# Optimization experiments

Measured on AMD Instinct MI355X. Metric: run time of the kernel, lower is better.

## Reference

```python
import jax, jax.numpy as jnp
import numpy as np

N, E, E_LBL = 50000, 800000, 200000
D_IN, H = 128, 128


def setup_inputs() -> dict:
    key = jax.random.key(0)
    ks = jax.random.split(key, 12)
    s = 0.05
    return {
        "x": jax.random.normal(ks[0], (N, D_IN), jnp.float32),
        "edge_index": jax.random.randint(ks[1], (2, E), 0, N, jnp.int64),
        "edge_label_index": jax.random.randint(ks[2], (2, E_LBL), 0, N, jnp.int64),
        "pre_w": jax.random.normal(ks[3], (D_IN, H), jnp.float32) * s,
        "pre_b": jax.random.normal(ks[4], (H,), jnp.float32) * s,
        "Wx": jax.random.normal(ks[5], (3, 2, H, H), jnp.float32) * s,  # gates z,r,h x cheb orders T0,T1
        "bx": jax.random.normal(ks[6], (3, H), jnp.float32) * s,
        "Wh": jax.random.normal(ks[7], (3, 2, H, H), jnp.float32) * s,
        "bh": jax.random.normal(ks[8], (3, H), jnp.float32) * s,
        "post_w": jax.random.normal(ks[9], (H, 2), jnp.float32) * s,
        "post_b": jax.random.normal(ks[10], (2,), jnp.float32) * s,
    }


def reference(x, edge_index, edge_label_index, pre_w, pre_b, Wx, bx, Wh, bh, post_w, post_b):
    n = x.shape[0]
    src, dst = edge_index[0], edge_index[1]

    # Scaled Chebyshev Laplacian (sym norm, lambda_max=2): L_hat = -D^{-1/2} A D^{-1/2}
    # (diagonal of L_hat is exactly 0, so only off-diagonal edge terms remain).
    deg = jax.ops.segment_sum(jnp.ones_like(src, dtype=x.dtype), src, num_segments=n)
    dinv = jnp.where(deg > 0, jax.lax.rsqrt(jnp.maximum(deg, 1.0)), 0.0)
    w = -(dinv[src] * dinv[dst])  # [E]

    def lap(v):  # L_hat @ v : gather src rows, weight, scatter-add at dst
        return jax.ops.segment_sum(w[:, None] * v[src], dst, num_segments=n)

    def cheb(v, Lv, W2, b):  # ChebConv K=2: T0(v)@W0 + T1(v)@W1 + b
        return v @ W2[0] + Lv @ W2[1] + b

    # pre: Linear(input_dim -> hidden)
    Xh = x @ pre_w + pre_b  # [N, H]
    LX = lap(Xh)

    # GConvGRU single step, H0 = 0
    Hc = jnp.zeros_like(Xh)
    LH = lap(Hc)
    Z = jax.nn.sigmoid(cheb(Xh, LX, Wx[0], bx[0]) + cheb(Hc, LH, Wh[0], bh[0]))
    R = jax.nn.sigmoid(cheb(Xh, LX, Wx[1], bx[1]) + cheb(Hc, LH, Wh[1], bh[1]))
    HR = Hc * R
    LHR = lap(HR)
    Ht = jnp.tanh(cheb(Xh, LX, Wx[2], bx[2]) + cheb(HR, LHR, Wh[2], bh[2]))
    Hc = Z * Hc + (1.0 - Z) * Ht

    h = jax.nn.relu(Hc)
    # link decoder: gather endpoints, hadamard, Linear(H->2), sum over logits
    hprod = h[edge_label_index[0]] * h[edge_label_index[1]]  # [E_lbl, H]
    out = hprod @ post_w + post_b  # [E_lbl, 2]
    return jnp.sum(out, axis=-1)  # [E_lbl]
```

## Files before the change

kernel.cpp:

```cpp
#include <hip/hip_runtime.h>
#include <math.h>


#define RND 2048
#define SORT_CAP 1536
#define CAPB 6144

typedef __attribute__((ext_vector_type(4))) float f32x4;
typedef __attribute__((ext_vector_type(8))) short short8;
typedef __attribute__((ext_vector_type(4))) unsigned u32x4;
typedef __attribute__((ext_vector_type(2))) unsigned u32x2;

static __device__ __forceinline__ unsigned short f2b(float f) {
  union { float f; unsigned u; } v; v.f = f;
  unsigned r = (v.u + 0x7fffu + ((v.u >> 16) & 1u)) >> 16;
  return (unsigned short)r;
}
static __device__ __forceinline__ float b2f(unsigned short s) {
  union { unsigned u; float f; } v; v.u = ((unsigned)s) << 16;
  return v.f;
}
static __device__ __forceinline__ unsigned f2e4m3(float f) {
  unsigned su = (__float_as_uint(f) >> 24) & 0x80u;
  float a = fminf(fabsf(f), 448.0f) * 0x1.0p-120f;
  unsigned u = __float_as_uint(a);
  u += 0x7FFFFu + ((u >> 20) & 1u);
  return su | ((u >> 20) & 0x7Fu);
}
static __device__ __forceinline__ float e4m32f(unsigned b) {
  unsigned u = ((b & 0x80u) << 24) | ((b & 0x7Fu) << 20);
  return __uint_as_float(u) * 0x1.0p120f;
}

__global__ __launch_bounds__(256) void prep_kernel(const float* __restrict__ pre_w, const float* __restrict__ Wx,
                                                   const float* __restrict__ bx, const float* __restrict__ bh,
                                                   const float* __restrict__ post_w, const float* __restrict__ post_b,
                                                   unsigned short* __restrict__ Bt1c, unsigned short* __restrict__ Btc2,
                                                   float* __restrict__ fb2, float* __restrict__ pwsum,
                                                   int* __restrict__ binPos) {
  int e = blockIdx.x * 256 + threadIdx.x;
  if (e < 512) binPos[e * 16] = (e & 255) * CAPB;
  if (e < 16384) {
    int kc = e >> 12, r = e & 4095, col = r >> 5, kk = r & 31;
    Bt1c[e] = f2b(pre_w[(kc * 32 + kk) * 128 + col]);
  }
  int e2 = e - 16384;
  if (e2 >= 0 && e2 < 65536) {
    int kc = e2 >> 13, r = e2 & 8191, cB = r >> 5, kk = r & 31;
    int k = kc * 32 + kk, half = k >> 7, ki = k & 127;
    int cb = cB >> 7, r7 = cB & 127, nw6 = r7 >> 6, u2 = r7 & 63;
    int g = (u2 >= 32) ? 2 : 0, hcol = cb * 64 + nw6 * 32 + (u2 & 31);
    Btc2[e2] = f2b(Wx[((g * 2 + half) * 128 + ki) * 128 + hcol]);
  }
  int e3 = e - (16384 + 65536);
  if (e3 >= 0 && e3 < 256) {
    int cB = e3;
    int cb = cB >> 7, r7 = cB & 127, nw6 = r7 >> 6, u2 = r7 & 63;
    int g = (u2 >= 32) ? 2 : 0, hcol = cb * 64 + nw6 * 32 + (u2 & 31);
    fb2[cB] = bx[g * 128 + hcol] + bh[g * 128 + hcol];
  }
  int e4 = e - (16384 + 65536 + 256);
  if (e4 >= 0 && e4 < 128) pwsum[e4] = post_w[2 * e4] + post_w[2 * e4 + 1];
  if (e4 == 128) pwsum[128] = post_b[0] + post_b[1];
}

union SMemU {
  struct { unsigned short As[128 * 40]; unsigned short Bs[128 * 40]; } g;
  struct { unsigned ent[RND]; int hist[256], lstart[256], lofs[256], gbase[256], wsum[4];
           unsigned char ebin[RND], sb[RND]; } s;
};

__global__ __launch_bounds__(256) void mega1_kernel(const float* __restrict__ x,
                                                    const unsigned short* __restrict__ Bt1c,
                                                    const float* __restrict__ pre_b,
                                                    unsigned short* __restrict__ Xq,
                                                    const int* __restrict__ ei, int* __restrict__ binPos,
                                                    unsigned* __restrict__ bins,
                                                    unsigned char* __restrict__ sbins,
                                                    int N, int E, int RB) {
  __shared__ SMemU sm;
  const int t = threadIdx.x;

  if ((int)blockIdx.x < RB) {
    unsigned short* As = sm.g.As;
    unsigned short* Bs = sm.g.Bs;
    const int r0 = blockIdx.x * 128;
    const int w = t >> 6, lane = t & 63;
    const int m = lane & 15, q = lane >> 4;
    const int mw = (w >> 1) * 64, nw = (w & 1) * 64;

    f32x4 acc[4][4];
#pragma unroll
    for (int i = 0; i < 4; ++i)
#pragma unroll
      for (int j = 0; j < 4; ++j) acc[i][j] = {0.f, 0.f, 0.f, 0.f};

    const int arow = t >> 1, aseg = t & 1;
    const bool arow_ok = (r0 + arow) < N;
    const float* asrc0 = &x[(size_t)(r0 + arow) * 128 + aseg * 16];

    float4 cav[4]; short8 cbv0, cbv1;
    {
      if (arow_ok) {
#pragma unroll
        for (int i = 0; i < 4; ++i) cav[i] = *(const float4*)(asrc0 + i * 4);
      } else {
#pragma unroll
        for (int i = 0; i < 4; ++i) cav[i] = make_float4(0.f, 0.f, 0.f, 0.f);
      }
      const char* src = (const char*)Bt1c + t * 32;
      cbv0 = *(const short8*)src;
      cbv1 = *(const short8*)(src + 16);
    }

    for (int kc = 0; kc < 4; ++kc) {
      __syncthreads();
      {
        short8 t0, t1;
#pragma unroll
        for (int i = 0; i < 2; ++i) {
          t0[i * 4 + 0] = (short)f2b(cav[i].x); t0[i * 4 + 1] = (short)f2b(cav[i].y);
          t0[i * 4 + 2] = (short)f2b(cav[i].z); t0[i * 4 + 3] = (short)f2b(cav[i].w);
          t1[i * 4 + 0] = (short)f2b(cav[i + 2].x); t1[i * 4 + 1] = (short)f2b(cav[i + 2].y);
          t1[i * 4 + 2] = (short)f2b(cav[i + 2].z); t1[i * 4 + 3] = (short)f2b(cav[i + 2].w);
        }
        *(short8*)&As[arow * 40 + aseg * 16] = t0;
        *(short8*)&As[arow * 40 + aseg * 16 + 8] = t1;
        int bcol = t >> 1, boff = (t & 1) * 16;
        *(short8*)&Bs[bcol * 40 + boff] = cbv0;
        *(short8*)&Bs[bcol * 40 + boff + 8] = cbv1;
      }
      float4 nav[4]; short8 nbv0, nbv1;
      if (kc < 3) {
        if (arow_ok) {
          const float* src = asrc0 + (kc + 1) * 32;
#pragma unroll
          for (int i = 0; i < 4; ++i) nav[i] = *(const float4*)(src + i * 4);
        } else {
#pragma unroll
          for (int i = 0; i < 4; ++i) nav[i] = make_float4(0.f, 0.f, 0.f, 0.f);
        }
        const char* src = (const char*)Bt1c + (size_t)(kc + 1) * 8192 + t * 32;
        nbv0 = *(const short8*)src;
        nbv1 = *(const short8*)(src + 16);
      }
      __syncthreads();
      short8 af[4], bf[4];
#pragma unroll
      for (int i = 0; i < 4; ++i) af[i] = *(const short8*)&As[(mw + i * 16 + m) * 40 + q * 8];
#pragma unroll
      for (int j = 0; j < 4; ++j) bf[j] = *(const short8*)&Bs[(nw + j * 16 + m) * 40 + q * 8];
#pragma unroll
      for (int i = 0; i < 4; ++i)
#pragma unroll
        for (int j = 0; j < 4; ++j)
          acc[i][j] = __builtin_amdgcn_mfma_f32_16x16x32_bf16(af[i], bf[j], acc[i][j], 0, 0, 0);
      if (kc < 3) {
#pragma unroll
        for (int i = 0; i < 4; ++i) cav[i] = nav[i];
        cbv0 = nbv0; cbv1 = nbv1;
      }
    }

#pragma unroll
    for (int i = 0; i < 4; ++i) {
      int rb2 = r0 + mw + i * 16 + q * 4;
#pragma unroll
      for (int j = 0; j < 4; ++j) {
        int col = nw + j * 16 + m;
        float bias = pre_b[col];
#pragma unroll
        for (int r = 0; r < 4; ++r) {
          int row = rb2 + r;
          if (row < N) Xq[(size_t)row * 128 + col] = f2b(acc[i][j][r] + bias);
        }
      }
    }
    return;
  }

  unsigned* ent = sm.s.ent;
  unsigned char* ebin = sm.s.ebin;
  unsigned char* sb = sm.s.sb;
  int* hist = sm.s.hist;
  int* lstart = sm.s.lstart;
  int* lofs = sm.s.lofs;
  int* gbase = sm.s.gbase;
  int* wsum = sm.s.wsum;
  const int sbid = (int)blockIdx.x - RB;
  const int snum = (int)gridDim.x - RB;
  const int w = t >> 6, lane = t & 63;
  for (long long base = (long long)sbid * RND; base < E; base += (long long)snum * RND) {
    int cnt = (int)(((long long)E - base < RND) ? (E - base) : RND);
    if (t < 256) hist[t] = 0;
    __syncthreads();
    int my_s[8], my_d[8];
#pragma unroll
    for (int u = 0; u < 8; ++u) {
      int i = u * 256 + t;
      my_s[u] = -1;
      if (i < cnt) {
        int idx = (int)base + i;
        my_s[u] = ei[idx];
        my_d[u] = ei[E + idx];
        atomicAdd(&hist[my_d[u] >> 8], 1);
      }
    }
    __syncthreads();
    {
      int h = hist[t];
      hist[t] = 0;
      int v = h;
#pragma unroll
      for (int dd = 1; dd < 64; dd <<= 1) { int uu = __shfl_up(v, dd); if (lane >= dd) v += uu; }
      if (lane == 63) wsum[w] = v;
      __syncthreads();
      int woff = 0;
#pragma unroll
      for (int ww = 0; ww < 3; ++ww) if (ww < w) woff += wsum[ww];
      int excl = v - h + woff;
      lstart[t] = excl; lofs[t] = excl;
      if (h > 0) gbase[t] = atomicAdd(&binPos[t * 16], h);
    }
    __syncthreads();
#pragma unroll
    for (int u = 0; u < 8; ++u) {
      if (my_s[u] >= 0) {
        int b = my_d[u] >> 8;
        int p = atomicAdd(&lofs[b], 1);
        ent[p] = (unsigned)my_s[u] | ((unsigned)(my_d[u] & 255) << 16);
        ebin[p] = (unsigned char)b;
        atomicAdd(&hist[my_s[u] >> 8], 1);
      }
    }
    __syncthreads();
    for (int i = t; i < cnt; i += 256) {
      int b = ebin[i];
      int pos = gbase[b] + (i - lstart[b]);
      if (pos < (b + 1) * CAPB) bins[pos] = ent[i];
    }
    __syncthreads();
    {
      int h = hist[t];
      int v = h;
#pragma unroll
      for (int dd = 1; dd < 64; dd <<= 1) { int uu = __shfl_up(v, dd); if (lane >= dd) v += uu; }
      if (lane == 63) wsum[w] = v;
      __syncthreads();
      int woff = 0;
#pragma unroll
      for (int ww = 0; ww < 3; ++ww) if (ww < w) woff += wsum[ww];
      int excl = v - h + woff;
      lstart[t] = excl; lofs[t] = excl;
      if (h > 0) gbase[t] = atomicAdd(&binPos[(256 + t) * 16], h);
    }
    __syncthreads();
#pragma unroll
    for (int u = 0; u < 8; ++u) {
      if (my_s[u] >= 0) {
        int b = my_s[u] >> 8;
        int p = atomicAdd(&lofs[b], 1);
        sb[p] = (unsigned char)(my_s[u] & 255);
        ebin[p] = (unsigned char)b;
      }
    }
    __syncthreads();
    for (int i = t; i < cnt; i += 256) {
      int b = ebin[i];
      int pos = gbase[b] + (i - lstart[b]);
      if (pos < (b + 1) * CAPB) sbins[pos] = sb[i];
    }
    __syncthreads();
  }
}

__global__ __launch_bounds__(512) void deghist_kernel(const unsigned char* __restrict__ sbins,
                                                      const int* __restrict__ binPos,
                                                      const unsigned short* __restrict__ Xq,
                                                      unsigned char* __restrict__ Xs,
                                                      float* __restrict__ dinvNeg, int N) {
  __shared__ int h[256];
  __shared__ float sdi[256];
  const int t = threadIdx.x;
  const int bin = blockIdx.x;
  if (t < 256) h[t] = 0;
  __syncthreads();
  int T2 = binPos[(256 + bin) * 16] - bin * CAPB;
  if (T2 > CAPB) T2 = CAPB;
  const unsigned char* __restrict__ p = sbins + (size_t)bin * CAPB;
  for (int i = t; i < T2; i += 512) atomicAdd(&h[p[i]], 1);
  __syncthreads();
  if (t < 256) {
    int node = bin * 256 + t;
    float di = h[t] > 0 ? rsqrtf((float)h[t]) : 0.0f;
    sdi[t] = di;
    if (node < N) dinvNeg[node] = -di;
  }
  __syncthreads();
  const int wv = t >> 6, lane = t & 63;
  const int g4 = lane >> 4, sl = lane & 15;
#pragma unroll
  for (int it = 0; it < 8; ++it) {
    int r = wv * 32 + it * 4 + g4;
    int rnode = bin * 256 + r;
    if (rnode < N) {
      float di_r = sdi[r];
      u32x4 v = *(const u32x4*)((const char*)Xq + (size_t)rnode * 256 + sl * 16);
      u32x2 o;
#pragma unroll
      for (int k = 0; k < 2; ++k) {
        unsigned w0 = 0;
#pragma unroll
        for (int j = 0; j < 2; ++j) {
          unsigned vv = v[k * 2 + j];
          union { unsigned u32; float f; } fl, fh;
          fl.u32 = vv << 16; fh.u32 = vv & 0xffff0000u;
          w0 |= f2e4m3(fl.f * di_r) << (j * 16);
          w0 |= f2e4m3(fh.f * di_r) << (j * 16 + 8);
        }
        o[k] = w0;
      }
      *(u32x2*)((char*)Xs + (size_t)rnode * 128 + sl * 8) = o;
    }
  }
}

__global__ __launch_bounds__(512) void lap_bin_kernel(const unsigned char* __restrict__ Xs,
                                                      unsigned short* __restrict__ LXc,
                                                      const unsigned* __restrict__ bins,
                                                      const int* __restrict__ binPos,
                                                      const float* __restrict__ dinvNeg, int N) {
  __shared__ unsigned eLDS[CAPB];
  __shared__ unsigned short sortS[SORT_CAP];
  __shared__ int hist[64], start[64], off[64];
  const int t = threadIdx.x;
  const int bin = blockIdx.x >> 2, qt = blockIdx.x & 3;
  const int lo = bin * CAPB;
  int T = binPos[bin * 16] - lo;
  if (T > CAPB) T = CAPB;
  const unsigned* __restrict__ ebase = &bins[lo];
  if (t < 64) hist[t] = 0;
  __syncthreads();
  for (int i = t; i < T; i += 512) {
    unsigned e = ebase[i];
    eLDS[i] = e;
    int dl = (e >> 16) & 255;
    if ((dl >> 6) == qt) atomicAdd(&hist[dl & 63], 1);
  }
  __syncthreads();
  if (t < 64) {
    int h = hist[t];
    int v = h;
#pragma unroll
    for (int d = 1; d < 64; d <<= 1) {
      int u = __shfl_up(v, d);
      if (t >= d) v += u;
    }
    start[t] = v - h;
    off[t] = v - h;
  }
  __syncthreads();
  for (int i = t; i < T; i += 512) {
    unsigned e = eLDS[i];
    int dl = (e >> 16) & 255;
    if ((dl >> 6) == qt) {
      int p = atomicAdd(&off[dl & 63], 1);
      if (p < SORT_CAP) sortS[p] = (unsigned short)(e & 0xFFFFu);
    }
  }
  __syncthreads();
  const int wv = t >> 6, lane = t & 63;
  const int g4 = lane >> 4, sl = lane & 15;
  for (int n = wv; n < 64; n += 8) {
    int node = bin * 256 + qt * 64 + n;
    if (node >= N) break;
    int st = start[n], cnum = hist[n];
    float acc[8] = {0.f, 0.f, 0.f, 0.f, 0.f, 0.f, 0.f, 0.f};
    for (int j = 0; j < cnum; j += 8) {
#pragma unroll
      for (int u = 0; u < 2; ++u) {
        int idx = j + u * 4 + g4;
        bool val = idx < cnum;
        int s = sortS[st + (val ? idx : 0)];
        u32x2 vv = *(const u32x2*)((const char*)Xs + (size_t)s * 128 + sl * 8);
        if (val) {
#pragma unroll
          for (int kk = 0; kk < 2; ++kk) {
            unsigned wv2 = vv[kk];
            acc[4 * kk + 0] += e4m32f(wv2 & 0xFFu);
            acc[4 * kk + 1] += e4m32f((wv2 >> 8) & 0xFFu);
            acc[4 * kk + 2] += e4m32f((wv2 >> 16) & 0xFFu);
            acc[4 * kk + 3] += e4m32f(wv2 >> 24);
          }
        }
      }
    }
#pragma unroll
    for (int k = 0; k < 8; ++k) {
      acc[k] += __shfl_xor(acc[k], 16);
      acc[k] += __shfl_xor(acc[k], 32);
    }
    if (g4 == 0) {
      float wd = dinvNeg[node];
      u32x4 o;
#pragma unroll
      for (int k = 0; k < 4; ++k)
        o[k] = (unsigned)f2b(acc[2 * k] * wd) | ((unsigned)f2b(acc[2 * k + 1] * wd) << 16);
      *(u32x4*)((char*)LXc + (size_t)node * 256 + sl * 16) = o;
    }
  }
}

__global__ __launch_bounds__(256) void gemm2_mfma(const unsigned short* __restrict__ Xq,
                                                  const unsigned short* __restrict__ LXc,
                                                  const unsigned short* __restrict__ Btc2,
                                                  const float* __restrict__ fb2,
                                                  unsigned short* __restrict__ hb, int N) {
  __shared__ unsigned short As[128 * 40];
  __shared__ unsigned short Bs[128 * 40];
  const int t = threadIdx.x;
  const int rb = blockIdx.x >> 1, cb = blockIdx.x & 1;
  const int r0 = rb * 128;
  const int w = t >> 6, lane = t & 63;
  const int m = lane & 15, q = lane >> 4;
  const int mw = (w >> 1) * 64, nw = (w & 1) * 64;

  f32x4 acc[4][4];
#pragma unroll
  for (int i = 0; i < 4; ++i)
#pragma unroll
    for (int j = 0; j < 4; ++j) acc[i][j] = {0.f, 0.f, 0.f, 0.f};

  const int arow = t >> 1;
  const int aoff = (t & 1) * 32;
  const char* aXq = (const char*)Xq + (size_t)(r0 + arow) * 256 + aoff;
  const char* aLX = (const char*)LXc + (size_t)(r0 + arow) * 256 + aoff;
  const char* bsrc0 = (const char*)Btc2 + (size_t)cb * 8192 + t * 32;

  short8 cav0, cav1, cbv0, cbv1;
  cav0 = *(const short8*)aXq;
  cav1 = *(const short8*)(aXq + 16);
  cbv0 = *(const short8*)bsrc0;
  cbv1 = *(const short8*)(bsrc0 + 16);

  for (int kc = 0; kc < 8; ++kc) {
    __syncthreads();
    *(short8*)&As[arow * 40 + (aoff >> 1)] = cav0;
    *(short8*)&As[arow * 40 + (aoff >> 1) + 8] = cav1;
    {
      int bcol = t >> 1, boff = (t & 1) * 16;
      *(short8*)&Bs[bcol * 40 + boff] = cbv0;
      *(short8*)&Bs[bcol * 40 + boff + 8] = cbv1;
    }
    short8 nav0, nav1, nbv0, nbv1;
    if (kc < 7) {
      int kn = kc + 1;
      const char* asrc = (kn < 4) ? (aXq + kn * 64) : (aLX + (kn - 4) * 64);
      nav0 = *(const short8*)asrc;
      nav1 = *(const short8*)(asrc + 16);
      const char* bsrc = bsrc0 + (size_t)kn * 16384;
      nbv0 = *(const short8*)bsrc;
      nbv1 = *(const short8*)(bsrc + 16);
    }
    __syncthreads();
    short8 af[4], bf[4];
#pragma unroll
    for (int i = 0; i < 4; ++i) af[i] = *(const short8*)&As[(mw + i * 16 + m) * 40 + q * 8];
#pragma unroll
    for (int j = 0; j < 4; ++j) bf[j] = *(const short8*)&Bs[(nw + j * 16 + m) * 40 + q * 8];
#pragma unroll
    for (int i = 0; i < 4; ++i)
#pragma unroll
      for (int j = 0; j < 4; ++j)
        acc[i][j] = __builtin_amdgcn_mfma_f32_16x16x32_bf16(af[i], bf[j], acc[i][j], 0, 0, 0);
    if (kc < 7) { cav0 = nav0; cav1 = nav1; cbv0 = nbv0; cbv1 = nbv1; }
  }

#pragma unroll
  for (int i = 0; i < 4; ++i) {
    int rbase = r0 + mw + i * 16 + q * 4;
#pragma unroll
    for (int jz = 0; jz < 2; ++jz) {
      int cBz = cb * 128 + nw + jz * 16 + m;
      int hc = cb * 64 + (nw >> 1) + jz * 16 + m;
      float bz = fb2[cBz], bt = fb2[cBz + 32];
#pragma unroll
      for (int r = 0; r < 4; ++r) {
        int row = rbase + r;
        if (row < N) {
          float zp = acc[i][jz][r] + bz;
          float tp = acc[i][jz + 2][r] + bt;
          float zs = 1.0f / (1.0f + __expf(-zp));
          float th = tanhf(tp);
          hb[(size_t)row * 128 + hc] = f2b(fmaxf((1.0f - zs) * th, 0.0f));
        }
      }
    }
  }
}

__global__ __launch_bounds__(256) void decoder_kernel(const unsigned short* __restrict__ hb,
                                                      const int* __restrict__ eli,
                                                      const float* __restrict__ pwsum, float* __restrict__ out, int M) {
  int t = threadIdx.x;
  int i = blockIdx.x * 16 + (t >> 4);
  int l = t & 15;
  if (i >= M) return;
  int a = eli[i], b = eli[M + i];
  int k = l * 8;
  short8 va = *(const short8*)&hb[(size_t)a * 128 + k];
  short8 vb = *(const short8*)&hb[(size_t)b * 128 + k];
  const float4* pwp = (const float4*)&pwsum[k];
  float4 p0 = pwp[0], p1 = pwp[1];
  float s = 0.0f;
  s += b2f((unsigned short)va[0]) * b2f((unsigned short)vb[0]) * p0.x;
  s += b2f((unsigned short)va[1]) * b2f((unsigned short)vb[1]) * p0.y;
  s += b2f((unsigned short)va[2]) * b2f((unsigned short)vb[2]) * p0.z;
  s += b2f((unsigned short)va[3]) * b2f((unsigned short)vb[3]) * p0.w;
  s += b2f((unsigned short)va[4]) * b2f((unsigned short)vb[4]) * p1.x;
  s += b2f((unsigned short)va[5]) * b2f((unsigned short)vb[5]) * p1.y;
  s += b2f((unsigned short)va[6]) * b2f((unsigned short)vb[6]) * p1.z;
  s += b2f((unsigned short)va[7]) * b2f((unsigned short)vb[7]) * p1.w;
#pragma unroll
  for (int off = 8; off; off >>= 1) s += __shfl_xor(s, off);
  if (l == 0) out[i] = s + pwsum[128];
}

extern "C" void kernel_launch(void* const* d_in, const int* in_sizes, int n_in,
                              void* d_out, int out_size, void* d_ws, size_t ws_size,
                              hipStream_t stream) {
  const float* x      = (const float*)d_in[0];
  const int*   ei     = (const int*)d_in[1];
  const int*   eli    = (const int*)d_in[2];
  const float* pre_w  = (const float*)d_in[3];
  const float* pre_b  = (const float*)d_in[4];
  const float* Wx     = (const float*)d_in[5];
  const float* bx     = (const float*)d_in[6];
  const float* bh     = (const float*)d_in[8];
  const float* post_w = (const float*)d_in[9];
  const float* post_b = (const float*)d_in[10];
  float* out = (float*)d_out;

  const int N = in_sizes[0] / 128;
  const int E = in_sizes[1] / 2;
  const int M = in_sizes[2] / 2;
  const int RB = (N + 127) / 128;
  const int NBIN = (N + 255) / 256;
  const int SCAT = (E + RND - 1) / RND;

  char* W = (char*)d_ws;
  size_t o = 0;
  float* dinvNeg = (float*)(W + o); o += (size_t)N * 4;
  o = (o + 255) & ~(size_t)255;
  int* binPos = (int*)(W + o);    o += 512 * 16 * 4;
  o = (o + 255) & ~(size_t)255;
  unsigned* bins = (unsigned*)(W + o); o += (size_t)NBIN * CAPB * 4;
  o = (o + 255) & ~(size_t)255;
  unsigned char* sbins = (unsigned char*)(W + o); o += (size_t)NBIN * CAPB;
  o = (o + 255) & ~(size_t)255;
  unsigned short* Xq = (unsigned short*)(W + o);  o += (size_t)RB * 128 * 256;
  unsigned char* Xs = (unsigned char*)(W + o);    o += (size_t)RB * 128 * 128;
  unsigned short* LXc = (unsigned short*)(W + o); o += (size_t)RB * 128 * 256;
  unsigned short* hb = (unsigned short*)(W + o);  o += (size_t)N * 256;
  unsigned short* Bt1c = (unsigned short*)(W + o); o += 32768;
  unsigned short* Btc2 = (unsigned short*)(W + o); o += 131072;
  float* fb2 = (float*)(W + o);  o += 1024;
  float* pwsum = (float*)(W + o); o += 768;

  prep_kernel<<<322, 256, 0, stream>>>(pre_w, Wx, bx, bh, post_w, post_b, Bt1c, Btc2, fb2, pwsum,
                                       binPos);
  mega1_kernel<<<RB + SCAT, 256, 0, stream>>>(x, Bt1c, pre_b, Xq, ei, binPos, bins, sbins, N, E, RB);
  deghist_kernel<<<NBIN, 512, 0, stream>>>(sbins, binPos, Xq, Xs, dinvNeg, N);
  lap_bin_kernel<<<NBIN * 4, 512, 0, stream>>>(Xs, LXc, bins, binPos, dinvNeg, N);
  gemm2_mfma<<<RB * 2, 256, 0, stream>>>(Xq, LXc, Btc2, fb2, hb, N);
  decoder_kernel<<<(M + 15) / 16, 256, 0, stream>>>(hb, eli, pwsum, out, M);
}
```

Baseline: 216.6 us.

## Use hardware fp8 pack/unpack and split Laplacian bins across eight blocks

Replaces the software e4m3 encode/decode helpers with the packed hardware conversion builtins (cvt_pk_fp8_f32 / cvt_pk_f32_fp8) in the degree-scaling and Laplacian gather kernels. It also splits each 256-node destination bin across 8 blocks of 32 nodes instead of 4 blocks of 64, doubling the grid for the gather kernel. The hardware conversion may differ slightly in saturation and rounding from the hand-written version. Each block still loads and scans the whole bin's edge list, so the finer split doubles that redundant scanning work.

```diff
diff --git a/kernel.cpp b/kernel.cpp
--- a/kernel.cpp
+++ b/kernel.cpp
@@ -7,6 +7,7 @@
 #define CAPB 6144
 
 typedef __attribute__((ext_vector_type(4))) float f32x4;
+typedef __attribute__((ext_vector_type(2))) float f32x2;
 typedef __attribute__((ext_vector_type(8))) short short8;
 typedef __attribute__((ext_vector_type(4))) unsigned u32x4;
 typedef __attribute__((ext_vector_type(2))) unsigned u32x2;
@@ -19,17 +20,6 @@
 static __device__ __forceinline__ float b2f(unsigned short s) {
   union { unsigned u; float f; } v; v.u = ((unsigned)s) << 16;
   return v.f;
-}
-static __device__ __forceinline__ unsigned f2e4m3(float f) {
-  unsigned su = (__float_as_uint(f) >> 24) & 0x80u;
-  float a = fminf(fabsf(f), 448.0f) * 0x1.0p-120f;
-  unsigned u = __float_as_uint(a);
-  u += 0x7FFFFu + ((u >> 20) & 1u);
-  return su | ((u >> 20) & 0x7Fu);
-}
-static __device__ __forceinline__ float e4m32f(unsigned b) {
-  unsigned u = ((b & 0x80u) << 24) | ((b & 0x7Fu) << 20);
-  return __uint_as_float(u) * 0x1.0p120f;
 }
 
 __global__ __launch_bounds__(256) void prep_kernel(const float* __restrict__ pre_w, const float* __restrict__ Wx,
@@ -306,20 +296,19 @@
     if (rnode < N) {
       float di_r = sdi[r];
       u32x4 v = *(const u32x4*)((const char*)Xq + (size_t)rnode * 256 + sl * 16);
-      u32x2 o;
-#pragma unroll
-      for (int k = 0; k < 2; ++k) {
-        unsigned w0 = 0;
-#pragma unroll
-        for (int j = 0; j < 2; ++j) {
-          unsigned vv = v[k * 2 + j];
-          union { unsigned u32; float f; } fl, fh;
-          fl.u32 = vv << 16; fh.u32 = vv & 0xffff0000u;
-          w0 |= f2e4m3(fl.f * di_r) << (j * 16);
-          w0 |= f2e4m3(fh.f * di_r) << (j * 16 + 8);
-        }
-        o[k] = w0;
-      }
+      float f[8];
+#pragma unroll
+      for (int j = 0; j < 4; ++j) {
+        union { unsigned u32; float ff; } fl, fh;
+        fl.u32 = v[j] << 16; fh.u32 = v[j] & 0xffff0000u;
+        f[2 * j] = fl.ff * di_r;
+        f[2 * j + 1] = fh.ff * di_r;
+      }
+      int w0 = __builtin_amdgcn_cvt_pk_fp8_f32(f[0], f[1], 0, false);
+      w0 = __builtin_amdgcn_cvt_pk_fp8_f32(f[2], f[3], w0, true);
+      int w1 = __builtin_amdgcn_cvt_pk_fp8_f32(f[4], f[5], 0, false);
+      w1 = __builtin_amdgcn_cvt_pk_fp8_f32(f[6], f[7], w1, true);
+      u32x2 o; o[0] = (unsigned)w0; o[1] = (unsigned)w1;
       *(u32x2*)((char*)Xs + (size_t)rnode * 128 + sl * 8) = o;
     }
   }
@@ -332,27 +321,27 @@
                                                       const float* __restrict__ dinvNeg, int N) {
   __shared__ unsigned eLDS[CAPB];
   __shared__ unsigned short sortS[SORT_CAP];
-  __shared__ int hist[64], start[64], off[64];
+  __shared__ int hist[32], start[32], off[32];
   const int t = threadIdx.x;
-  const int bin = blockIdx.x >> 2, qt = blockIdx.x & 3;
+  const int bin = blockIdx.x >> 3, qt = blockIdx.x & 7;
   const int lo = bin * CAPB;
   int T = binPos[bin * 16] - lo;
   if (T > CAPB) T = CAPB;
   const unsigned* __restrict__ ebase = &bins[lo];
-  if (t < 64) hist[t] = 0;
+  if (t < 32) hist[t] = 0;
   __syncthreads();
   for (int i = t; i < T; i += 512) {
     unsigned e = ebase[i];
     eLDS[i] = e;
     int dl = (e >> 16) & 255;
-    if ((dl >> 6) == qt) atomicAdd(&hist[dl & 63], 1);
-  }
-  __syncthreads();
-  if (t < 64) {
+    if ((dl >> 5) == qt) atomicAdd(&hist[dl & 31], 1);
+  }
+  __syncthreads();
+  if (t < 32) {
     int h = hist[t];
     int v = h;
 #pragma unroll
-    for (int d = 1; d < 64; d <<= 1) {
+    for (int d = 1; d < 32; d <<= 1) {
       int u = __shfl_up(v, d);
       if (t >= d) v += u;
     }
@@ -363,16 +352,16 @@
   for (int i = t; i < T; i += 512) {
     unsigned e = eLDS[i];
     int dl = (e >> 16) & 255;
-    if ((dl >> 6) == qt) {
-      int p = atomicAdd(&off[dl & 63], 1);
+    if ((dl >> 5) == qt) {
+      int p = atomicAdd(&off[dl & 31], 1);
       if (p < SORT_CAP) sortS[p] = (unsigned short)(e & 0xFFFFu);
     }
   }
   __syncthreads();
   const int wv = t >> 6, lane = t & 63;
   const int g4 = lane >> 4, sl = lane & 15;
-  for (int n = wv; n < 64; n += 8) {
-    int node = bin * 256 + qt * 64 + n;
+  for (int n = wv; n < 32; n += 8) {
+    int node = bin * 256 + qt * 32 + n;
     if (node >= N) break;
     int st = start[n], cnum = hist[n];
     float acc[8] = {0.f, 0.f, 0.f, 0.f, 0.f, 0.f, 0.f, 0.f};
@@ -384,14 +373,12 @@
         int s = sortS[st + (val ? idx : 0)];
         u32x2 vv = *(const u32x2*)((const char*)Xs + (size_t)s * 128 + sl * 8);
         if (val) {
-#pragma unroll
-          for (int kk = 0; kk < 2; ++kk) {
-            unsigned wv2 = vv[kk];
-            acc[4 * kk + 0] += e4m32f(wv2 & 0xFFu);
-            acc[4 * kk + 1] += e4m32f((wv2 >> 8) & 0xFFu);
-            acc[4 * kk + 2] += e4m32f((wv2 >> 16) & 0xFFu);
-            acc[4 * kk + 3] += e4m32f(wv2 >> 24);
-          }
+          f32x2 p0 = __builtin_amdgcn_cvt_pk_f32_fp8((int)vv[0], false);
+          f32x2 p1 = __builtin_amdgcn_cvt_pk_f32_fp8((int)vv[0], true);
+          f32x2 p2 = __builtin_amdgcn_cvt_pk_f32_fp8((int)vv[1], false);
+          f32x2 p3 = __builtin_amdgcn_cvt_pk_f32_fp8((int)vv[1], true);
+          acc[0] += p0[0]; acc[1] += p0[1]; acc[2] += p1[0]; acc[3] += p1[1];
+          acc[4] += p2[0]; acc[5] += p2[1]; acc[6] += p3[0]; acc[7] += p3[1];
         }
       }
     }
@@ -571,7 +558,7 @@
                                        binPos);
   mega1_kernel<<<RB + SCAT, 256, 0, stream>>>(x, Bt1c, pre_b, Xq, ei, binPos, bins, sbins, N, E, RB);
   deghist_kernel<<<NBIN, 512, 0, stream>>>(sbins, binPos, Xq, Xs, dinvNeg, N);
-  lap_bin_kernel<<<NBIN * 4, 512, 0, stream>>>(Xs, LXc, bins, binPos, dinvNeg, N);
+  lap_bin_kernel<<<NBIN * 8, 512, 0, stream>>>(Xs, LXc, bins, binPos, dinvNeg, N);
   gemm2_mfma<<<RB * 2, 256, 0, stream>>>(Xq, LXc, Btc2, fb2, hb, N);
   decoder_kernel<<<(M + 15) / 16, 256, 0, stream>>>(hb, eli, pwsum, out, M);
 }
```

New measurement: 200.5 us. 1.08x faster.
